# Kernel optimization log

Measured on AMD Instinct MI355X. Metric: run time of the kernel, lower is better.

## Reference

```python
import jax, jax.numpy as jnp
import numpy as np

ALPHA = 0.2  # LeakyReLU negative slope
NEG_INF = -9e15


def setup_inputs() -> dict:
    key = jax.random.key(0)
    ks = jax.random.split(key, 6)
    B, N, F_IN, F_OUT = 4, 1024, 64, 64
    h = jax.random.normal(ks[0], (B, N, F_IN), dtype=jnp.float32)
    adj = jax.random.randint(ks[1], (B, N, N), 0, 2, dtype=jnp.int32)
    lin_w = jax.random.normal(ks[2], (F_OUT, F_IN), dtype=jnp.float32) * (1.0 / np.sqrt(F_IN))
    lin_b = jax.random.normal(ks[3], (F_OUT,), dtype=jnp.float32) * 0.02
    W_w = jax.random.normal(ks[4], (F_OUT, 2 * F_OUT), dtype=jnp.float32) * (1.0 / np.sqrt(2 * F_OUT))
    a = jax.random.normal(ks[5], (F_OUT, 1), dtype=jnp.float32) * (1.414 / np.sqrt(F_OUT))
    return {"h": h, "adj": adj, "lin_w": lin_w, "lin_b": lin_b, "W_w": W_w, "a": a}


def reference(h, adj, lin_w, lin_b, W_w, a):
    F_OUT = lin_w.shape[0]
    # h' = Linear(h): (B, N, F_OUT)
    hp = jnp.einsum('bni,oi->bno', h, lin_w) + lin_b
    # W @ concat(h_i, h_j) == h_i @ W1^T + h_j @ W2^T  (same math, no 2F concat)
    W1, W2 = W_w[:, :F_OUT], W_w[:, F_OUT:]
    u = jnp.einsum('bnf,of->bno', hp, W1)  # source/row term   (B, N, F_OUT)
    v = jnp.einsum('bnf,of->bno', hp, W2)  # target/col term   (B, N, F_OUT)
    s = u[:, :, None, :] + v[:, None, :, :]        # (B, N, N, F_OUT)
    s = jnp.where(s > 0, s, ALPHA * s)             # LeakyReLU
    e = jnp.einsum('bijf,f->bij', s, a[:, 0])      # (B, N, N)
    e = jnp.where(adj > 0, e, NEG_INF)
    attention = jax.nn.softmax(e, axis=2)
    h_prime = jnp.einsum('bij,bjf->bif', attention, hp)
    return jax.nn.elu(h_prime)
```

## Files before the change

kernel.cpp:

```cpp
#include <hip/hip_runtime.h>
#include <hip/hip_bf16.h>
#include <math.h>

constexpr int B = 4;
constexpr int N = 1024;
constexpr float NEGINF = -9000000000000000.0f;

__global__ __launch_bounds__(256) void gat_prep(
    const float* __restrict__ h, const float* __restrict__ lin_w,
    const float* __restrict__ lin_b, const float* __restrict__ W_w,
    const float* __restrict__ a_g,
    float* __restrict__ hp, float* __restrict__ u_out, float* __restrict__ vT,
    float* __restrict__ au_out, float* __restrict__ av_out) {
  __shared__ float hs[64 * 34];
  __shared__ float wl[64 * 68];
  __shared__ float w1[64 * 68];
  __shared__ float w2[64 * 68];
  __shared__ float hpT[64 * 34];
  __shared__ float vt_s[64 * 33];
  __shared__ float ared[2][32 * 17];
  __shared__ float lb_s[64], a_s[64];

  const int b = blockIdx.x >> 5;
  const int n0 = (blockIdx.x & 31) << 5;
  const int tid = threadIdx.x;

  for (int idx = tid; idx < 2048; idx += 256) {
    const int r = idx >> 6, c = idx & 63;
    hs[c * 34 + r] = h[((b << 10) + n0 + r) * 64 + c];
  }
  for (int idx = tid; idx < 4096; idx += 256) {
    const int o = idx >> 6, f = idx & 63;
    wl[f * 68 + o] = lin_w[idx];
    w1[f * 68 + o] = W_w[o * 128 + f];
    w2[f * 68 + o] = W_w[o * 128 + 64 + f];
  }
  if (tid < 64) { lb_s[tid] = lin_b[tid]; a_s[tid] = a_g[tid]; }
  __syncthreads();

  const int tf = tid & 15, tn = tid >> 4;
  float ahp[2][4];
#pragma unroll
  for (int q = 0; q < 2; ++q)
#pragma unroll
    for (int r = 0; r < 4; ++r) ahp[q][r] = lb_s[tf * 4 + r];
#pragma unroll 4
  for (int k = 0; k < 64; ++k) {
    const float2 h2 = *(const float2*)&hs[k * 34 + tn * 2];
    const float4 l4 = *(const float4*)&wl[k * 68 + tf * 4];
    const float hv[2] = {h2.x, h2.y};
    const float lv[4] = {l4.x, l4.y, l4.z, l4.w};
#pragma unroll
    for (int q = 0; q < 2; ++q)
#pragma unroll
      for (int r = 0; r < 4; ++r) ahp[q][r] = fmaf(hv[q], lv[r], ahp[q][r]);
  }
#pragma unroll
  for (int q = 0; q < 2; ++q) {
    const int row = (b << 10) + n0 + tn * 2 + q;
    *(float4*)&hp[row * 64 + tf * 4] =
        make_float4(ahp[q][0], ahp[q][1], ahp[q][2], ahp[q][3]);
#pragma unroll
    for (int r = 0; r < 4; ++r) hpT[(tf * 4 + r) * 34 + tn * 2 + q] = ahp[q][r];
  }
  __syncthreads();

  float aU[2][4] = {}, aV[2][4] = {};
#pragma unroll 4
  for (int k = 0; k < 64; ++k) {
    const float2 h2 = *(const float2*)&hpT[k * 34 + tn * 2];
    const float4 u4 = *(const float4*)&w1[k * 68 + tf * 4];
    const float4 v4 = *(const float4*)&w2[k * 68 + tf * 4];
    const float hv[2] = {h2.x, h2.y};
    const float uv[4] = {u4.x, u4.y, u4.z, u4.w};
    const float vv[4] = {v4.x, v4.y, v4.z, v4.w};
#pragma unroll
    for (int q = 0; q < 2; ++q)
#pragma unroll
      for (int r = 0; r < 4; ++r) {
        aU[q][r] = fmaf(hv[q], uv[r], aU[q][r]);
        aV[q][r] = fmaf(hv[q], vv[r], aV[q][r]);
      }
  }
#pragma unroll
  for (int q = 0; q < 2; ++q) {
    const int row = (b << 10) + n0 + tn * 2 + q;
    *(float4*)&u_out[row * 64 + tf * 4] =
        make_float4(aU[q][0], aU[q][1], aU[q][2], aU[q][3]);
  }
  float aup[2] = {0.f, 0.f}, avp[2] = {0.f, 0.f};
#pragma unroll
  for (int q = 0; q < 2; ++q)
#pragma unroll
    for (int r = 0; r < 4; ++r) {
      vt_s[(tf * 4 + r) * 33 + tn * 2 + q] = aV[q][r];
      aup[q] = fmaf(a_s[tf * 4 + r], aU[q][r], aup[q]);
      avp[q] = fmaf(a_s[tf * 4 + r], aV[q][r], avp[q]);
    }
#pragma unroll
  for (int q = 0; q < 2; ++q) {
    ared[0][(tn * 2 + q) * 17 + tf] = aup[q];
    ared[1][(tn * 2 + q) * 17 + tf] = avp[q];
  }
  __syncthreads();
  for (int idx = tid; idx < 2048; idx += 256) {
    const int f = idx >> 5, n = idx & 31;
    vT[(((b << 6) + f) << 10) + n0 + n] = vt_s[f * 33 + n];
  }
  if (tid < 64) {
    const int which = tid >> 5, row = tid & 31;
    float s2 = 0.f;
#pragma unroll
    for (int t = 0; t < 16; ++t) s2 += ared[which][row * 17 + t];
    if (which == 0) au_out[(b << 10) + n0 + row] = s2;
    else av_out[(b << 10) + n0 + row] = s2;
  }
}

__global__ __launch_bounds__(256) void gat_attn(
    const float* __restrict__ u_g, const float* __restrict__ vT,
    const float* __restrict__ hp, const int* __restrict__ adj,
    const float* __restrict__ a_g, const float* __restrict__ au_g,
    const float* __restrict__ av_g, float* __restrict__ out) {
  __shared__ float p_s[4 * 1024];
  __shared__ float u_s[64 * 4];
  __shared__ float a_s[64];
  __shared__ float au_s[4];
  __shared__ float wred[4][4];
  __shared__ float wsum[4][4];
  __shared__ float rinv_s[4];

  const int b = blockIdx.x >> 8;
  const int i0 = (blockIdx.x & 255) << 2;
  const int tid = threadIdx.x;
  const int lane = tid & 63, w = tid >> 6;
  const int j0 = tid << 2;

  if (tid < 64) a_s[tid] = a_g[tid];
  if (tid < 4) au_s[tid] = au_g[(b << 10) + i0 + tid];
  {
    const int i = tid >> 6, f = tid & 63;
    u_s[f * 4 + i] = u_g[((b << 10) + i0 + i) * 64 + f];
  }
  __syncthreads();

  float e[4][4];
#pragma unroll
  for (int i = 0; i < 4; ++i)
#pragma unroll
    for (int k = 0; k < 4; ++k) e[i][k] = 0.f;

  const float* vb = vT + ((b << 6) << 10);
#pragma unroll 4
  for (int f = 0; f < 64; ++f) {
    const float af = a_s[f];
    const float4 v4 = *(const float4*)&vb[(f << 10) + j0];
    const float4 u4 = *(const float4*)&u_s[f * 4];
    const float uu[4] = {u4.x, u4.y, u4.z, u4.w};
    const float vv[4] = {v4.x, v4.y, v4.z, v4.w};
#pragma unroll
    for (int i = 0; i < 4; ++i)
#pragma unroll
      for (int k = 0; k < 4; ++k)
        e[i][k] = fmaf(af, fabsf(uu[i] + vv[k]), e[i][k]);
  }
  const float4 av4 = *(const float4*)&av_g[(b << 10) + j0];
  const float avv[4] = {0.6f * av4.x, 0.6f * av4.y, 0.6f * av4.z, 0.6f * av4.w};
  float au6[4];
#pragma unroll
  for (int i = 0; i < 4; ++i) au6[i] = 0.6f * au_s[i];
  const int* adjb = adj + ((((b << 10) + i0)) << 10) + j0;
#pragma unroll
  for (int i = 0; i < 4; ++i) {
    const int4 ad = *(const int4*)&adjb[i << 10];
    const int adv[4] = {ad.x, ad.y, ad.z, ad.w};
#pragma unroll
    for (int k = 0; k < 4; ++k) {
      const float ev = fmaf(0.4f, e[i][k], au6[i] + avv[k]);
      e[i][k] = adv[k] > 0 ? ev : NEGINF;
    }
  }

#pragma unroll
  for (int i = 0; i < 4; ++i) {
    float mm = fmaxf(fmaxf(e[i][0], e[i][1]), fmaxf(e[i][2], e[i][3]));
#pragma unroll
    for (int off = 32; off; off >>= 1) mm = fmaxf(mm, __shfl_xor(mm, off));
    if (lane == 0) wred[w][i] = mm;
  }
  __syncthreads();
#pragma unroll
  for (int i = 0; i < 4; ++i) {
    const float mi = fmaxf(fmaxf(wred[0][i], wred[1][i]),
                           fmaxf(wred[2][i], wred[3][i]));
#pragma unroll
    for (int k = 0; k < 4; ++k) e[i][k] = __expf(e[i][k] - mi);
    float ss = e[i][0] + e[i][1] + e[i][2] + e[i][3];
#pragma unroll
    for (int off = 32; off; off >>= 1) ss += __shfl_xor(ss, off);
    if (lane == 0) wsum[w][i] = ss;
  }
  __syncthreads();
  if (tid < 4)
    rinv_s[tid] = 1.0f / (wsum[0][tid] + wsum[1][tid] + wsum[2][tid] + wsum[3][tid]);
#pragma unroll
  for (int i = 0; i < 4; ++i)
    *(float4*)&p_s[(i << 10) + j0] = make_float4(e[i][0], e[i][1], e[i][2], e[i][3]);
  __syncthreads();

  const int fl = tid & 63, g = tid >> 6;
  float acc[4] = {0.f, 0.f, 0.f, 0.f};
  const float* hpb = hp + (b << 16);
  for (int jj = g << 8; jj < (g << 8) + 256; jj += 4) {
    const float4 p0 = *(const float4*)&p_s[jj];
    const float4 p1 = *(const float4*)&p_s[1024 + jj];
    const float4 p2 = *(const float4*)&p_s[2048 + jj];
    const float4 p3 = *(const float4*)&p_s[3072 + jj];
    float hv[4];
#pragma unroll
    for (int t = 0; t < 4; ++t) hv[t] = hpb[((jj + t) << 6) + fl];
    acc[0] += p0.x * hv[0] + p0.y * hv[1] + p0.z * hv[2] + p0.w * hv[3];
    acc[1] += p1.x * hv[0] + p1.y * hv[1] + p1.z * hv[2] + p1.w * hv[3];
    acc[2] += p2.x * hv[0] + p2.y * hv[1] + p2.z * hv[2] + p2.w * hv[3];
    acc[3] += p3.x * hv[0] + p3.y * hv[1] + p3.z * hv[2] + p3.w * hv[3];
  }
  __syncthreads();
  float* red = p_s;
#pragma unroll
  for (int i = 0; i < 4; ++i) red[(((g << 2) + i) << 6) + fl] = acc[i];
  __syncthreads();
  {
    const int i = tid >> 6, f = tid & 63;
    float r = red[((i) << 6) + f] + red[((4 + i) << 6) + f] +
              red[((8 + i) << 6) + f] + red[((12 + i) << 6) + f];
    r *= rinv_s[i];
    out[((b << 10) + i0 + i) * 64 + f] = r > 0.f ? r : expm1f(r);
  }
}

extern "C" void kernel_launch(void* const* d_in, const int* in_sizes, int n_in,
                              void* d_out, int out_size, void* d_ws, size_t ws_size,
                              hipStream_t stream) {
  const float* h = (const float*)d_in[0];
  const int* adj = (const int*)d_in[1];
  const float* lin_w = (const float*)d_in[2];
  const float* lin_b = (const float*)d_in[3];
  const float* W_w = (const float*)d_in[4];
  const float* a = (const float*)d_in[5];
  float* outp = (float*)d_out;

  float* ws = (float*)d_ws;
  float* hp = ws;
  float* u = ws + 262144;
  float* vT = ws + 524288;
  float* au = ws + 786432;
  float* av = ws + 790528;

  gat_prep<<<dim3(128), dim3(256), 0, stream>>>(h, lin_w, lin_b, W_w, a,
                                                hp, u, vT, au, av);
  gat_attn<<<dim3(1024), dim3(256), 0, stream>>>(u, vT, hp, adj, a, au, av, outp);
}
```

Baseline: 119.3 us.

## Halve prep tile rows to double grid, prefetch adj early in attention

The prep kernel now gives each block 16 rows instead of 32 and launches 256 blocks, so each thread computes one row. This spreads the small linear and projection GEMMs across more CUs. The attention kernel issues the adjacency and av loads before the first barrier so their latency overlaps the feature loop, and it raises unroll factors on the inner loops. In exchange, each prep block reloads the full weight matrices for half as many rows, and the prefetched int4 values add register pressure.

```diff
diff --git a/kernel.cpp b/kernel.cpp
--- a/kernel.cpp
+++ b/kernel.cpp
@@ -12,22 +12,23 @@
     const float* __restrict__ a_g,
     float* __restrict__ hp, float* __restrict__ u_out, float* __restrict__ vT,
     float* __restrict__ au_out, float* __restrict__ av_out) {
-  __shared__ float hs[64 * 34];
+  __shared__ float hs[64 * 18];
   __shared__ float wl[64 * 68];
   __shared__ float w1[64 * 68];
   __shared__ float w2[64 * 68];
-  __shared__ float hpT[64 * 34];
-  __shared__ float vt_s[64 * 33];
-  __shared__ float ared[2][32 * 17];
+  __shared__ float hpT[64 * 18];
+  __shared__ float vt_s[64 * 17];
+  __shared__ float ared[2][16 * 17];
   __shared__ float lb_s[64], a_s[64];
 
-  const int b = blockIdx.x >> 5;
-  const int n0 = (blockIdx.x & 31) << 5;
+  const int b = blockIdx.x >> 6;
+  const int n0 = (blockIdx.x & 63) << 4;
   const int tid = threadIdx.x;
 
-  for (int idx = tid; idx < 2048; idx += 256) {
+  if (tid < 64) { lb_s[tid] = lin_b[tid]; a_s[tid] = a_g[tid]; }
+  for (int idx = tid; idx < 1024; idx += 256) {
     const int r = idx >> 6, c = idx & 63;
-    hs[c * 34 + r] = h[((b << 10) + n0 + r) * 64 + c];
+    hs[c * 18 + r] = h[((b << 10) + n0 + r) * 64 + c];
   }
   for (int idx = tid; idx < 4096; idx += 256) {
     const int o = idx >> 6, f = idx & 63;
@@ -35,85 +36,64 @@
     w1[f * 68 + o] = W_w[o * 128 + f];
     w2[f * 68 + o] = W_w[o * 128 + 64 + f];
   }
-  if (tid < 64) { lb_s[tid] = lin_b[tid]; a_s[tid] = a_g[tid]; }
   __syncthreads();
 
   const int tf = tid & 15, tn = tid >> 4;
-  float ahp[2][4];
-#pragma unroll
-  for (int q = 0; q < 2; ++q)
-#pragma unroll
-    for (int r = 0; r < 4; ++r) ahp[q][r] = lb_s[tf * 4 + r];
-#pragma unroll 4
+  float ahp[4];
+#pragma unroll
+  for (int r = 0; r < 4; ++r) ahp[r] = lb_s[tf * 4 + r];
+#pragma unroll 8
   for (int k = 0; k < 64; ++k) {
-    const float2 h2 = *(const float2*)&hs[k * 34 + tn * 2];
+    const float hv = hs[k * 18 + tn];
     const float4 l4 = *(const float4*)&wl[k * 68 + tf * 4];
-    const float hv[2] = {h2.x, h2.y};
-    const float lv[4] = {l4.x, l4.y, l4.z, l4.w};
-#pragma unroll
-    for (int q = 0; q < 2; ++q)
-#pragma unroll
-      for (int r = 0; r < 4; ++r) ahp[q][r] = fmaf(hv[q], lv[r], ahp[q][r]);
-  }
-#pragma unroll
-  for (int q = 0; q < 2; ++q) {
-    const int row = (b << 10) + n0 + tn * 2 + q;
-    *(float4*)&hp[row * 64 + tf * 4] =
-        make_float4(ahp[q][0], ahp[q][1], ahp[q][2], ahp[q][3]);
-#pragma unroll
-    for (int r = 0; r < 4; ++r) hpT[(tf * 4 + r) * 34 + tn * 2 + q] = ahp[q][r];
-  }
-  __syncthreads();
-
-  float aU[2][4] = {}, aV[2][4] = {};
-#pragma unroll 4
+    ahp[0] = fmaf(hv, l4.x, ahp[0]);
+    ahp[1] = fmaf(hv, l4.y, ahp[1]);
+    ahp[2] = fmaf(hv, l4.z, ahp[2]);
+    ahp[3] = fmaf(hv, l4.w, ahp[3]);
+  }
+  const int row = (b << 10) + n0 + tn;
+  *(float4*)&hp[row * 64 + tf * 4] = make_float4(ahp[0], ahp[1], ahp[2], ahp[3]);
+#pragma unroll
+  for (int r = 0; r < 4; ++r) hpT[(tf * 4 + r) * 18 + tn] = ahp[r];
+  __syncthreads();
+
+  float aU[4] = {0.f, 0.f, 0.f, 0.f}, aV[4] = {0.f, 0.f, 0.f, 0.f};
+#pragma unroll 8
   for (int k = 0; k < 64; ++k) {
-    const float2 h2 = *(const float2*)&hpT[k * 34 + tn * 2];
+    const float hv = hpT[k * 18 + tn];
     const float4 u4 = *(const float4*)&w1[k * 68 + tf * 4];
     const float4 v4 = *(const float4*)&w2[k * 68 + tf * 4];
-    const float hv[2] = {h2.x, h2.y};
-    const float uv[4] = {u4.x, u4.y, u4.z, u4.w};
-    const float vv[4] = {v4.x, v4.y, v4.z, v4.w};
-#pragma unroll
-    for (int q = 0; q < 2; ++q)
-#pragma unroll
-      for (int r = 0; r < 4; ++r) {
-        aU[q][r] = fmaf(hv[q], uv[r], aU[q][r]);
-        aV[q][r] = fmaf(hv[q], vv[r], aV[q][r]);
-      }
-  }
-#pragma unroll
-  for (int q = 0; q < 2; ++q) {
-    const int row = (b << 10) + n0 + tn * 2 + q;
-    *(float4*)&u_out[row * 64 + tf * 4] =
-        make_float4(aU[q][0], aU[q][1], aU[q][2], aU[q][3]);
-  }
-  float aup[2] = {0.f, 0.f}, avp[2] = {0.f, 0.f};
-#pragma unroll
-  for (int q = 0; q < 2; ++q)
-#pragma unroll
-    for (int r = 0; r < 4; ++r) {
-      vt_s[(tf * 4 + r) * 33 + tn * 2 + q] = aV[q][r];
-      aup[q] = fmaf(a_s[tf * 4 + r], aU[q][r], aup[q]);
-      avp[q] = fmaf(a_s[tf * 4 + r], aV[q][r], avp[q]);
-    }
-#pragma unroll
-  for (int q = 0; q < 2; ++q) {
-    ared[0][(tn * 2 + q) * 17 + tf] = aup[q];
-    ared[1][(tn * 2 + q) * 17 + tf] = avp[q];
-  }
-  __syncthreads();
-  for (int idx = tid; idx < 2048; idx += 256) {
-    const int f = idx >> 5, n = idx & 31;
-    vT[(((b << 6) + f) << 10) + n0 + n] = vt_s[f * 33 + n];
-  }
-  if (tid < 64) {
-    const int which = tid >> 5, row = tid & 31;
+    aU[0] = fmaf(hv, u4.x, aU[0]);
+    aU[1] = fmaf(hv, u4.y, aU[1]);
+    aU[2] = fmaf(hv, u4.z, aU[2]);
+    aU[3] = fmaf(hv, u4.w, aU[3]);
+    aV[0] = fmaf(hv, v4.x, aV[0]);
+    aV[1] = fmaf(hv, v4.y, aV[1]);
+    aV[2] = fmaf(hv, v4.z, aV[2]);
+    aV[3] = fmaf(hv, v4.w, aV[3]);
+  }
+  *(float4*)&u_out[row * 64 + tf * 4] = make_float4(aU[0], aU[1], aU[2], aU[3]);
+  float aup = 0.f, avp = 0.f;
+#pragma unroll
+  for (int r = 0; r < 4; ++r) {
+    vt_s[(tf * 4 + r) * 17 + tn] = aV[r];
+    aup = fmaf(a_s[tf * 4 + r], aU[r], aup);
+    avp = fmaf(a_s[tf * 4 + r], aV[r], avp);
+  }
+  ared[0][tn * 17 + tf] = aup;
+  ared[1][tn * 17 + tf] = avp;
+  __syncthreads();
+  for (int idx = tid; idx < 1024; idx += 256) {
+    const int f = idx >> 4, n = idx & 15;
+    vT[(((b << 6) + f) << 10) + n0 + n] = vt_s[f * 17 + n];
+  }
+  if (tid < 32) {
+    const int which = tid >> 4, rr = tid & 15;
     float s2 = 0.f;
 #pragma unroll
-    for (int t = 0; t < 16; ++t) s2 += ared[which][row * 17 + t];
-    if (which == 0) au_out[(b << 10) + n0 + row] = s2;
-    else av_out[(b << 10) + n0 + row] = s2;
+    for (int t = 0; t < 16; ++t) s2 += ared[which][rr * 17 + t];
+    if (which == 0) au_out[(b << 10) + n0 + rr] = s2;
+    else av_out[(b << 10) + n0 + rr] = s2;
   }
 }
 
@@ -142,6 +122,13 @@
     const int i = tid >> 6, f = tid & 63;
     u_s[f * 4 + i] = u_g[((b << 10) + i0 + i) * 64 + f];
   }
+
+  const int* adjb = adj + (((b << 10) + i0) << 10) + j0;
+  int4 ad4[4];
+#pragma unroll
+  for (int i = 0; i < 4; ++i) ad4[i] = *(const int4*)&adjb[i << 10];
+  const float4 av4 = *(const float4*)&av_g[(b << 10) + j0];
+
   __syncthreads();
 
   float e[4][4];
@@ -151,7 +138,7 @@
     for (int k = 0; k < 4; ++k) e[i][k] = 0.f;
 
   const float* vb = vT + ((b << 6) << 10);
-#pragma unroll 4
+#pragma unroll 8
   for (int f = 0; f < 64; ++f) {
     const float af = a_s[f];
     const float4 v4 = *(const float4*)&vb[(f << 10) + j0];
@@ -164,16 +151,13 @@
       for (int k = 0; k < 4; ++k)
         e[i][k] = fmaf(af, fabsf(uu[i] + vv[k]), e[i][k]);
   }
-  const float4 av4 = *(const float4*)&av_g[(b << 10) + j0];
   const float avv[4] = {0.6f * av4.x, 0.6f * av4.y, 0.6f * av4.z, 0.6f * av4.w};
   float au6[4];
 #pragma unroll
   for (int i = 0; i < 4; ++i) au6[i] = 0.6f * au_s[i];
-  const int* adjb = adj + ((((b << 10) + i0)) << 10) + j0;
 #pragma unroll
   for (int i = 0; i < 4; ++i) {
-    const int4 ad = *(const int4*)&adjb[i << 10];
-    const int adv[4] = {ad.x, ad.y, ad.z, ad.w};
+    const int adv[4] = {ad4[i].x, ad4[i].y, ad4[i].z, ad4[i].w};
 #pragma unroll
     for (int k = 0; k < 4; ++k) {
       const float ev = fmaf(0.4f, e[i][k], au6[i] + avv[k]);
@@ -211,6 +195,7 @@
   const int fl = tid & 63, g = tid >> 6;
   float acc[4] = {0.f, 0.f, 0.f, 0.f};
   const float* hpb = hp + (b << 16);
+#pragma unroll 4
   for (int jj = g << 8; jj < (g << 8) + 256; jj += 4) {
     const float4 p0 = *(const float4*)&p_s[jj];
     const float4 p1 = *(const float4*)&p_s[1024 + jj];
@@ -256,7 +241,7 @@
   float* au = ws + 786432;
   float* av = ws + 790528;
 
-  gat_prep<<<dim3(128), dim3(256), 0, stream>>>(h, lin_w, lin_b, W_w, a,
+  gat_prep<<<dim3(256), dim3(256), 0, stream>>>(h, lin_w, lin_b, W_w, a,
                                                 hp, u, vT, au, av);
   gat_attn<<<dim3(1024), dim3(256), 0, stream>>>(u, vT, hp, adj, a, au, av, outp);
 }
```

New measurement: 124.2 us. +4.1%, slower.
